# Performance work log

Hardware: AMD Instinct MI355X
Metric: run time of the kernel (lower is better)

Reference implementation:

```python
import jax, jax.numpy as jnp
import numpy as np

T = 2048          # tokens (single causal prefill sequence)
H = 4096          # hidden_size
NH = 32           # num query heads
NKV = 8           # num kv heads (GQA)
HD = H // NH      # head_dim = 128
ROPE_THETA = 500000.0
Q_SIZE = NH * HD
KV_SIZE = NKV * HD


def setup_inputs() -> dict:
    key = jax.random.key(0)
    k1, k2, k3 = jax.random.split(key, 3)
    return {
        "positions": jnp.arange(T, dtype=jnp.int32),
        "hidden_states": jax.random.normal(k1, (T, H), dtype=jnp.float32) * 0.02,
        "w_qkv": jax.random.normal(k2, (H, Q_SIZE + 2 * KV_SIZE), dtype=jnp.float32) * (1.0 / np.sqrt(H)),
        "w_o": jax.random.normal(k3, (Q_SIZE, H), dtype=jnp.float32) * (1.0 / np.sqrt(Q_SIZE)),
    }


def _apply_rope(x, positions):
    # x: [T, heads, HD]; neox-style (non-interleaved) RoPE as in get_rope
    half = HD // 2
    inv_freq = 1.0 / (ROPE_THETA ** (jnp.arange(0, half, dtype=jnp.float32) / half * 1.0))
    # note: standard llama uses arange(0, HD, 2)/HD == arange(half)/half
    freqs = positions.astype(jnp.float32)[:, None] * inv_freq[None, :]   # [T, half]
    cos = jnp.cos(freqs)[:, None, :]  # [T, 1, half]
    sin = jnp.sin(freqs)[:, None, :]
    x1, x2 = x[..., :half], x[..., half:]
    return jnp.concatenate([x1 * cos - x2 * sin, x2 * cos + x1 * sin], axis=-1).astype(x.dtype)


def reference(positions, hidden_states, w_qkv, w_o):
    # qkv_proj (no bias)
    qkv = hidden_states @ w_qkv                               # [T, 6144]
    q, k, v = jnp.split(qkv, [Q_SIZE, Q_SIZE + KV_SIZE], axis=-1)
    q = q.reshape(T, NH, HD)
    k = k.reshape(T, NKV, HD)
    v = v.reshape(T, NKV, HD)

    # fused RoPE on q and k (k would be written rotated into the KV cache)
    q = _apply_rope(q, positions)
    k = _apply_rope(k, positions)

    # GQA: expand kv heads to query heads
    group = NH // NKV
    k_rep = jnp.repeat(k, group, axis=1)                      # [T, NH, HD]
    v_rep = jnp.repeat(v, group, axis=1)

    scale = HD ** -0.5
    scores = jnp.einsum('qhd,shd->hqs', q, k_rep) * scale     # [NH, T, T]
    causal = jnp.tril(jnp.ones((T, T), dtype=bool))
    scores = jnp.where(causal[None], scores, jnp.finfo(scores.dtype).min)
    probs = jax.nn.softmax(scores, axis=-1)
    attn = jnp.einsum('hqs,shd->qhd', probs, v_rep)           # [T, NH, HD]

    out = attn.reshape(T, Q_SIZE) @ w_o                       # o_proj
    return out
```

## Files before the change

kernel.cpp:

```cpp
#include <hip/hip_runtime.h>
#include <cstdint>
#include <cstddef>

#define T_SEQ 2048
#define H_DIM 4096
#define NH 32
#define NKV 8
#define HD 128
#define QKV_N 6144
#define Q_SIZE 4096
#define KV_SIZE 1024

typedef __attribute__((ext_vector_type(8))) short bf16x8;
typedef __attribute__((ext_vector_type(4))) short short4v;
typedef __attribute__((ext_vector_type(4))) float f32x4;

__device__ __forceinline__ short f2bf(float f) {
  union { float f; uint32_t u; } v; v.f = f;
  uint32_t r = v.u + 0x7fffu + ((v.u >> 16) & 1u);
  return (short)(r >> 16);
}

__device__ __forceinline__ void gload_lds16(const void* g, void* l) {
  __builtin_amdgcn_global_load_lds((const __attribute__((address_space(1))) void*)g,
                                   (__attribute__((address_space(3))) void*)l,
                                   16, 0, 0);
}

__global__ __launch_bounds__(256) void cvt_bf16_kernel(const float* __restrict__ in,
                                                       short* __restrict__ out, int n4) {
  int i = blockIdx.x * 256 + threadIdx.x;
  if (i < n4) {
    float4 v = ((const float4*)in)[i];
    short4v s;
    s.x = f2bf(v.x); s.y = f2bf(v.y); s.z = f2bf(v.z); s.w = f2bf(v.w);
    ((short4v*)out)[i] = s;
  }
}

__global__ __launch_bounds__(256) void transpose_cvt_kernel(const float* __restrict__ in,
                                                            short* __restrict__ out,
                                                            int rows, int cols) {
  __shared__ float tile[32][33];
  int bx = blockIdx.x * 32;
  int by = blockIdx.y * 32;
  int x = threadIdx.x, y = threadIdx.y;
#pragma unroll
  for (int i = 0; i < 32; i += 8)
    tile[y + i][x] = in[(size_t)(by + y + i) * cols + bx + x];
  __syncthreads();
#pragma unroll
  for (int i = 0; i < 32; i += 8)
    out[(size_t)(bx + y + i) * rows + by + x] = f2bf(tile[x][y + i]);
}

#define BARRIER() do { __builtin_amdgcn_s_barrier(); \
                       __builtin_amdgcn_sched_barrier(0); \
                       asm volatile("" ::: "memory"); } while (0)
#define VMCNT4() asm volatile("s_waitcnt vmcnt(4)" ::: "memory")
#define PRIO1 __builtin_amdgcn_s_setprio(1)
#define PRIO0 __builtin_amdgcn_s_setprio(0)

#define LDA_HALF(BASE, MH) do { \
  _Pragma("unroll") \
  for (int m_ = 0; m_ < 4; ++m_) { \
    _Pragma("unroll") \
    for (int ks_ = 0; ks_ < 2; ++ks_) { \
      int row_ = arow + (MH) * 64 + m_ * 16 + l16; \
      aF[m_][ks_] = *(const bf16x8*)((BASE) + row_ * 64 + (((ks_ * 4 + quad) ^ (row_ & 7)) << 3)); \
    } } } while (0)

#define LDB_HALF(BASE, NH, DST) do { \
  _Pragma("unroll") \
  for (int n_ = 0; n_ < 2; ++n_) { \
    _Pragma("unroll") \
    for (int ks_ = 0; ks_ < 2; ++ks_) { \
      int row_ = brow + (NH) * 32 + n_ * 16 + l16; \
      (DST)[n_][ks_] = *(const bf16x8*)((BASE) + row_ * 64 + (((ks_ * 4 + quad) ^ (row_ & 7)) << 3)); \
    } } } while (0)

#define MMQ(MH, NH, BF) do { \
  _Pragma("unroll") \
  for (int m_ = 0; m_ < 4; ++m_) { \
    _Pragma("unroll") \
    for (int n_ = 0; n_ < 2; ++n_) { \
      _Pragma("unroll") \
      for (int ks_ = 0; ks_ < 2; ++ks_) \
        acc[(MH) * 4 + m_][(NH) * 2 + n_] = __builtin_amdgcn_mfma_f32_16x16x32_bf16( \
            aF[m_][ks_], (BF)[n_][ks_], acc[(MH) * 4 + m_][(NH) * 2 + n_], 0, 0, 0); \
    } } } while (0)

__device__ __forceinline__ void stage_half(const short* __restrict__ src, int ldk,
                                           short* dst, int half, int tid) {
#pragma unroll
  for (int q = 0; q < 2; ++q) {
    int cc = half * 1024 + q * 512 + tid;
    int row = cc >> 3, cq = cc & 7;
    gload_lds16(src + (size_t)row * ldk + ((cq ^ (row & 7)) << 3), dst + cc * 8);
  }
}

__global__ __launch_bounds__(512, 1) void gemm_bt256_kernel(const short* __restrict__ A,
                                                            const short* __restrict__ Bt,
                                                            float* __restrict__ C,
                                                            int M, int N, int K) {
  __shared__ short lds[65536];
  short* As0 = lds;
  short* Bs0 = lds + 16384;
  short* As1 = lds + 32768;
  short* Bs1 = lds + 49152;
  int tid = threadIdx.x;
  int w = tid >> 6, lane = tid & 63;
  int quad = lane >> 4, l16 = lane & 15;
  int wr = w >> 2, wc = w & 3;
  int arow = wr * 128, brow = wc * 64;
  int bm = blockIdx.y * 256, bn = blockIdx.x * 256;
  const short* Asrc = A + (size_t)bm * K;
  const short* Bsrc = Bt + (size_t)bn * K;
  int NT = K >> 6, NI = NT >> 1;

  f32x4 acc[8][4] = {};
  bf16x8 aF[4][2], b0F[2][2], b1F[2][2];

  stage_half(Asrc, K, As0, 0, tid);
  stage_half(Asrc, K, As0, 1, tid);
  stage_half(Bsrc, K, Bs0, 0, tid);
  stage_half(Bsrc, K, Bs0, 1, tid);
  stage_half(Bsrc + 64, K, Bs1, 0, tid);
  stage_half(Bsrc + 64, K, Bs1, 1, tid);
  VMCNT4();
  BARRIER();

#pragma unroll 1
  for (int i = 0; i < NI; ++i) {
    const short* a1 = Asrc + (size_t)(2 * i + 1) * 64;
    int kt2 = 2 * i + 2; if (kt2 > NT - 1) kt2 = NT - 1;
    int kt3 = 2 * i + 3; if (kt3 > NT - 1) kt3 = NT - 1;
    const short* a2 = Asrc + (size_t)kt2 * 64;
    const short* b2 = Bsrc + (size_t)kt2 * 64;
    const short* b3 = Bsrc + (size_t)kt3 * 64;

    LDA_HALF(As0, 0);
    LDB_HALF(Bs0, 0, b0F);
    stage_half(a1, K, As1, 0, tid);
    BARRIER();
    PRIO1; MMQ(0, 0, b0F); PRIO0;
    BARRIER();
    LDB_HALF(Bs0, 1, b1F);
    stage_half(a1, K, As1, 1, tid);
    BARRIER();
    PRIO1; MMQ(0, 1, b1F); PRIO0;
    BARRIER();
    LDA_HALF(As0, 1);
    stage_half(b2, K, Bs0, 0, tid);
    BARRIER();
    PRIO1; MMQ(1, 1, b1F); PRIO0;
    BARRIER();
    stage_half(b2, K, Bs0, 1, tid);
    BARRIER();
    PRIO1; MMQ(1, 0, b0F); PRIO0;
    VMCNT4();
    BARRIER();
    LDA_HALF(As1, 0);
    LDB_HALF(Bs1, 0, b0F);
    stage_half(a2, K, As0, 0, tid);
    BARRIER();
    PRIO1; MMQ(0, 0, b0F); PRIO0;
    BARRIER();
    LDB_HALF(Bs1, 1, b1F);
    stage_half(a2, K, As0, 1, tid);
    BARRIER();
    PRIO1; MMQ(0, 1, b1F); PRIO0;
    BARRIER();
    LDA_HALF(As1, 1);
    stage_half(b3, K, Bs1, 0, tid);
    BARRIER();
    PRIO1; MMQ(1, 1, b1F); PRIO0;
    BARRIER();
    stage_half(b3, K, Bs1, 1, tid);
    BARRIER();
    PRIO1; MMQ(1, 0, b0F); PRIO0;
    VMCNT4();
    BARRIER();
  }
  asm volatile("s_waitcnt vmcnt(0)" ::: "memory");

#pragma unroll
  for (int mi = 0; mi < 8; ++mi)
#pragma unroll
    for (int ni = 0; ni < 4; ++ni) {
      int r0 = bm + arow + mi * 16 + quad * 4;
      int c0 = bn + brow + ni * 16 + l16;
#pragma unroll
      for (int r = 0; r < 4; ++r)
        C[(size_t)(r0 + r) * N + c0] = acc[mi][ni][r];
    }
}

__global__ __launch_bounds__(256) void rope_kernel(const float* __restrict__ qkv,
                                                   const int* __restrict__ positions,
                                                   short* __restrict__ qb,
                                                   short* __restrict__ kb) {
  int t = blockIdx.x;
  int hh = blockIdx.y * 4 + (threadIdx.x >> 6);
  int j = threadIdx.x & 63;
  float pos = (float)positions[t];
  float f = pos * exp2f(-(float)j * 0.29580575889569017f);
  float c = cosf(f), sn = sinf(f);
  size_t rowbase = (size_t)t * QKV_N;
  int coloff = (hh < NH) ? hh * HD : Q_SIZE + (hh - NH) * HD;
  float x1 = qkv[rowbase + coloff + j];
  float x2 = qkv[rowbase + coloff + j + 64];
  float o1 = x1 * c - x2 * sn;
  float o2 = x2 * c + x1 * sn;
  const float scale2 = 0.08838834764831845f * 1.4426950408889634f;
  short* dst;
  if (hh < NH) {
    o1 *= scale2; o2 *= scale2;
    dst = qb + ((size_t)hh * T_SEQ + t) * HD;
  } else {
    dst = kb + ((size_t)(hh - NH) * T_SEQ + t) * HD;
  }
  dst[j] = f2bf(o1);
  dst[j + 64] = f2bf(o2);
}

__global__ __launch_bounds__(256) void transpose_v_kernel(const float* __restrict__ qkv,
                                                          short* __restrict__ vt) {
  __shared__ float tile[32][33];
  int bx = blockIdx.x * 32;
  int by = blockIdx.y * 32;
  int x = threadIdx.x, y = threadIdx.y;
#pragma unroll
  for (int i = 0; i < 32; i += 8)
    tile[y + i][x] = qkv[(size_t)(by + y + i) * QKV_N + (Q_SIZE + KV_SIZE) + bx + x];
  __syncthreads();
#pragma unroll
  for (int i = 0; i < 32; i += 8)
    vt[(size_t)(bx + y + i) * T_SEQ + by + x] = f2bf(tile[x][y + i]);
}

#define PS_STR 72
__global__ __launch_bounds__(256, 2) void flash_kernel(const short* __restrict__ qb,
                                                       const short* __restrict__ kb,
                                                       const short* __restrict__ vt,
                                                       short* __restrict__ attn) {
  __shared__ short Ks[64 * 128];
  __shared__ short Vs[128 * 64];
  __shared__ short Ps[8][16 * PS_STR];
  int c = (int)gridDim.x - 1 - (int)blockIdx.x;
  int h = blockIdx.y;
  int kvh = h >> 2;
  int tid = threadIdx.x;
  int w = tid >> 6, lane = tid & 63;
  int quad = lane >> 4, l16 = lane & 15;
  int qrow0w = c * 128 + w * 32;

  const short* kbh = kb + (size_t)kvh * T_SEQ * HD;
  const short* vth = vt + (size_t)kvh * HD * T_SEQ;

  bf16x8 qf[2][4];
#pragma unroll
  for (int g = 0; g < 2; ++g) {
    const short* qbase = qb + ((size_t)h * T_SEQ + qrow0w + g * 16 + l16) * HD + quad * 8;
#pragma unroll
    for (int dk = 0; dk < 4; ++dk) qf[g][dk] = *(const bf16x8*)(qbase + dk * 32);
  }
  f32x4 o[2][8] = {};
  float lp[2] = {0.0f, 0.0f};

  int ktmax_blk = 2 * c + 2;
  int ktmax_w = 2 * c + 1 + (w >> 1);

  for (int kt = 0; kt < ktmax_blk; ++kt) {
    int kpos0 = kt * 64;
    __syncthreads();
#pragma unroll
    for (int p4 = 0; p4 < 4; ++p4) {
      int e = p4 * 256 + tid;
      int kr = e >> 4, kp = e & 15;
      gload_lds16(kbh + (size_t)(kpos0 + kr) * HD + ((kp ^ (kr & 7)) * 8), Ks + e * 8);
      int vd = e >> 3, vp = e & 7;
      gload_lds16(vth + (size_t)vd * T_SEQ + kpos0 + ((vp ^ (vd & 7)) * 8), Vs + e * 8);
    }
    __syncthreads();
    if (kt >= ktmax_w) continue;

    f32x4 s[2][4] = {};
#pragma unroll
    for (int mi = 0; mi < 4; ++mi) {
      int kr = mi * 16 + l16;
      const short* kfb = Ks + kr * 128;
      int sw = kr & 7;
#pragma unroll
      for (int dk = 0; dk < 4; ++dk) {
        bf16x8 kf = *(const bf16x8*)(kfb + (((dk * 4 + quad) ^ sw) * 8));
        s[0][mi] = __builtin_amdgcn_mfma_f32_16x16x32_bf16(kf, qf[0][dk], s[0][mi], 0, 0, 0);
        s[1][mi] = __builtin_amdgcn_mfma_f32_16x16x32_bf16(kf, qf[1][dk], s[1][mi], 0, 0, 0);
      }
    }
#pragma unroll
    for (int g = 0; g < 2; ++g) {
      int qr = qrow0w + g * 16 + l16;
      bool need_mask = (kpos0 + 63 > qrow0w + g * 16);
#pragma unroll
      for (int mi = 0; mi < 4; ++mi) {
        float p0, p1, p2, p3;
        if (need_mask) {
          int kp = kpos0 + mi * 16 + quad * 4;
          p0 = exp2f((kp + 0 > qr) ? -1e30f : s[g][mi][0]);
          p1 = exp2f((kp + 1 > qr) ? -1e30f : s[g][mi][1]);
          p2 = exp2f((kp + 2 > qr) ? -1e30f : s[g][mi][2]);
          p3 = exp2f((kp + 3 > qr) ? -1e30f : s[g][mi][3]);
        } else {
          p0 = exp2f(s[g][mi][0]); p1 = exp2f(s[g][mi][1]);
          p2 = exp2f(s[g][mi][2]); p3 = exp2f(s[g][mi][3]);
        }
        lp[g] += p0 + p1 + p2 + p3;
        short4v pk;
        pk.x = f2bf(p0); pk.y = f2bf(p1); pk.z = f2bf(p2); pk.w = f2bf(p3);
        *(short4v*)(&Ps[w * 2 + g][l16 * PS_STR + mi * 16 + quad * 4]) = pk;
      }
    }
#pragma unroll
    for (int kf2 = 0; kf2 < 2; ++kf2) {
      bf16x8 pf0 = *(const bf16x8*)(&Ps[w * 2 + 0][l16 * PS_STR + kf2 * 32 + quad * 8]);
      bf16x8 pf1 = *(const bf16x8*)(&Ps[w * 2 + 1][l16 * PS_STR + kf2 * 32 + quad * 8]);
#pragma unroll
      for (int ni = 0; ni < 8; ++ni) {
        int vd = ni * 16 + l16;
        bf16x8 vf = *(const bf16x8*)(Vs + vd * 64 + (((kf2 * 4 + quad) ^ (vd & 7)) * 8));
        o[0][ni] = __builtin_amdgcn_mfma_f32_16x16x32_bf16(vf, pf0, o[0][ni], 0, 0, 0);
        o[1][ni] = __builtin_amdgcn_mfma_f32_16x16x32_bf16(vf, pf1, o[1][ni], 0, 0, 0);
      }
    }
  }
#pragma unroll
  for (int g = 0; g < 2; ++g) {
    float lt = lp[g];
    lt += __shfl_xor(lt, 16, 64);
    lt += __shfl_xor(lt, 32, 64);
    float rl = 1.0f / lt;
    short* dst = attn + (size_t)(qrow0w + g * 16 + l16) * Q_SIZE + h * HD + quad * 4;
#pragma unroll
    for (int ni = 0; ni < 8; ++ni) {
      short4v ov;
      ov.x = f2bf(o[g][ni][0] * rl); ov.y = f2bf(o[g][ni][1] * rl);
      ov.z = f2bf(o[g][ni][2] * rl); ov.w = f2bf(o[g][ni][3] * rl);
      *(short4v*)(dst + ni * 16) = ov;
    }
  }
}

extern "C" void kernel_launch(void* const* d_in, const int* in_sizes, int n_in,
                              void* d_out, int out_size, void* d_ws, size_t ws_size,
                              hipStream_t stream) {
  const int* positions = (const int*)d_in[0];
  const float* hidden  = (const float*)d_in[1];
  const float* w_qkv   = (const float*)d_in[2];
  const float* w_o     = (const float*)d_in[3];
  float* out = (float*)d_out;

  char* p = (char*)d_ws;
  short* hA    = (short*)p;               short* attn = hA;
  p += (size_t)T_SEQ * H_DIM * 2;
  short* wqkvT = (short*)p;
  p += (size_t)QKV_N * H_DIM * 2;
  float* qkv   = (float*)p;               short* woT = (short*)p;
  short* qb = wqkvT;
  short* kb = qb + (size_t)NH * T_SEQ * HD;
  short* vt = kb + (size_t)NKV * T_SEQ * HD;

  cvt_bf16_kernel<<<dim3(T_SEQ * H_DIM / 4 / 256), 256, 0, stream>>>(hidden, hA, T_SEQ * H_DIM / 4);
  transpose_cvt_kernel<<<dim3(QKV_N / 32, H_DIM / 32), dim3(32, 8), 0, stream>>>(w_qkv, wqkvT, H_DIM, QKV_N);
  gemm_bt256_kernel<<<dim3(QKV_N / 256, T_SEQ / 256), 512, 0, stream>>>(hA, wqkvT, qkv, T_SEQ, QKV_N, H_DIM);
  rope_kernel<<<dim3(T_SEQ, (NH + NKV) / 4), 256, 0, stream>>>(qkv, positions, qb, kb);
  transpose_v_kernel<<<dim3(KV_SIZE / 32, T_SEQ / 32), dim3(32, 8), 0, stream>>>(qkv, vt);
  transpose_cvt_kernel<<<dim3(H_DIM / 32, H_DIM / 32), dim3(32, 8), 0, stream>>>(w_o, woT, H_DIM, H_DIM);
  flash_kernel<<<dim3(T_SEQ / 128, NH), 256, 0, stream>>>(qb, kb, vt, attn);
  gemm_bt256_kernel<<<dim3(H_DIM / 256, T_SEQ / 256), 512, 0, stream>>>(attn, woT, out, T_SEQ, H_DIM, H_DIM);
}
```

Measured before the change: 543.0 us.

## Split-K the o_proj GEMM with atomics and widen weight transpose tiles

The o_proj GEMM grid had only 128 blocks (16x8) on a device with far more CUs. It now splits K in two, zeroes the output first and accumulates with float atomicAdd, doubling the block count. The weight transpose-convert kernel also moves to 64x64 tiles with float4 loads and 16-byte bf16 stores. The trade-off is an extra zeroing pass and atomic write traffic, plus non-deterministic summation order.

```diff
diff --git a/kernel.cpp b/kernel.cpp
--- a/kernel.cpp
+++ b/kernel.cpp
@@ -38,20 +38,41 @@
   }
 }
 
-__global__ __launch_bounds__(256) void transpose_cvt_kernel(const float* __restrict__ in,
-                                                            short* __restrict__ out,
-                                                            int rows, int cols) {
-  __shared__ float tile[32][33];
-  int bx = blockIdx.x * 32;
-  int by = blockIdx.y * 32;
-  int x = threadIdx.x, y = threadIdx.y;
-#pragma unroll
-  for (int i = 0; i < 32; i += 8)
-    tile[y + i][x] = in[(size_t)(by + y + i) * cols + bx + x];
+__global__ __launch_bounds__(256) void zero_f4_kernel(float* __restrict__ p, int n4) {
+  int i = blockIdx.x * 256 + threadIdx.x;
+  int stride = gridDim.x * 256;
+  float4 z = {0.f, 0.f, 0.f, 0.f};
+  for (; i < n4; i += stride) ((float4*)p)[i] = z;
+}
+
+__global__ __launch_bounds__(256) void transpose_cvt64_kernel(const float* __restrict__ in,
+                                                              short* __restrict__ out,
+                                                              int rows, int cols) {
+  __shared__ float tile[64][65];
+  int bx = blockIdx.x * 64;
+  int by = blockIdx.y * 64;
+  int t = threadIdx.x;
+  int lr = t >> 4;
+  int lc4 = t & 15;
+#pragma unroll
+  for (int p = 0; p < 4; ++p) {
+    int r = p * 16 + lr;
+    float4 v = *(const float4*)(in + (size_t)(by + r) * cols + bx + lc4 * 4);
+    tile[r][lc4 * 4 + 0] = v.x; tile[r][lc4 * 4 + 1] = v.y;
+    tile[r][lc4 * 4 + 2] = v.z; tile[r][lc4 * 4 + 3] = v.w;
+  }
   __syncthreads();
-#pragma unroll
-  for (int i = 0; i < 32; i += 8)
-    out[(size_t)(bx + y + i) * rows + by + x] = f2bf(tile[x][y + i]);
+  int w = t >> 6, l = t & 63;
+  int colg = l >> 3;
+  int rseg = (l & 7) * 8;
+#pragma unroll
+  for (int p = 0; p < 2; ++p) {
+    int col = (p * 4 + w) * 8 + colg;
+    bf16x8 r8;
+#pragma unroll
+    for (int i = 0; i < 8; ++i) r8[i] = f2bf(tile[rseg + i][col]);
+    *(bf16x8*)(out + (size_t)(bx + col) * rows + by + rseg) = r8;
+  }
 }
 
 #define BARRIER() do { __builtin_amdgcn_s_barrier(); \
@@ -103,7 +124,8 @@
 __global__ __launch_bounds__(512, 1) void gemm_bt256_kernel(const short* __restrict__ A,
                                                             const short* __restrict__ Bt,
                                                             float* __restrict__ C,
-                                                            int M, int N, int K) {
+                                                            int M, int N, int K,
+                                                            int klen) {
   __shared__ short lds[65536];
   short* As0 = lds;
   short* Bs0 = lds + 16384;
@@ -115,9 +137,10 @@
   int wr = w >> 2, wc = w & 3;
   int arow = wr * 128, brow = wc * 64;
   int bm = blockIdx.y * 256, bn = blockIdx.x * 256;
-  const short* Asrc = A + (size_t)bm * K;
-  const short* Bsrc = Bt + (size_t)bn * K;
-  int NT = K >> 6, NI = NT >> 1;
+  int k0 = blockIdx.z * klen;
+  const short* Asrc = A + (size_t)bm * K + k0;
+  const short* Bsrc = Bt + (size_t)bn * K + k0;
+  int NT = klen >> 6, NI = NT >> 1;
 
   f32x4 acc[8][4] = {};
   bf16x8 aF[4][2], b0F[2][2], b1F[2][2];
@@ -185,16 +208,29 @@
   }
   asm volatile("s_waitcnt vmcnt(0)" ::: "memory");
 
-#pragma unroll
-  for (int mi = 0; mi < 8; ++mi)
-#pragma unroll
-    for (int ni = 0; ni < 4; ++ni) {
-      int r0 = bm + arow + mi * 16 + quad * 4;
-      int c0 = bn + brow + ni * 16 + l16;
-#pragma unroll
-      for (int r = 0; r < 4; ++r)
-        C[(size_t)(r0 + r) * N + c0] = acc[mi][ni][r];
-    }
+  if (gridDim.z > 1) {
+#pragma unroll
+    for (int mi = 0; mi < 8; ++mi)
+#pragma unroll
+      for (int ni = 0; ni < 4; ++ni) {
+        int r0 = bm + arow + mi * 16 + quad * 4;
+        int c0 = bn + brow + ni * 16 + l16;
+#pragma unroll
+        for (int r = 0; r < 4; ++r)
+          atomicAdd(&C[(size_t)(r0 + r) * N + c0], acc[mi][ni][r]);
+      }
+  } else {
+#pragma unroll
+    for (int mi = 0; mi < 8; ++mi)
+#pragma unroll
+      for (int ni = 0; ni < 4; ++ni) {
+        int r0 = bm + arow + mi * 16 + quad * 4;
+        int c0 = bn + brow + ni * 16 + l16;
+#pragma unroll
+        for (int r = 0; r < 4; ++r)
+          C[(size_t)(r0 + r) * N + c0] = acc[mi][ni][r];
+      }
+  }
 }
 
 __global__ __launch_bounds__(256) void rope_kernel(const float* __restrict__ qkv,
@@ -372,11 +408,12 @@
   short* vt = kb + (size_t)NKV * T_SEQ * HD;
 
   cvt_bf16_kernel<<<dim3(T_SEQ * H_DIM / 4 / 256), 256, 0, stream>>>(hidden, hA, T_SEQ * H_DIM / 4);
-  transpose_cvt_kernel<<<dim3(QKV_N / 32, H_DIM / 32), dim3(32, 8), 0, stream>>>(w_qkv, wqkvT, H_DIM, QKV_N);
-  gemm_bt256_kernel<<<dim3(QKV_N / 256, T_SEQ / 256), 512, 0, stream>>>(hA, wqkvT, qkv, T_SEQ, QKV_N, H_DIM);
+  transpose_cvt64_kernel<<<dim3(QKV_N / 64, H_DIM / 64), 256, 0, stream>>>(w_qkv, wqkvT, H_DIM, QKV_N);
+  gemm_bt256_kernel<<<dim3(QKV_N / 256, T_SEQ / 256, 1), 512, 0, stream>>>(hA, wqkvT, qkv, T_SEQ, QKV_N, H_DIM, H_DIM);
   rope_kernel<<<dim3(T_SEQ, (NH + NKV) / 4), 256, 0, stream>>>(qkv, positions, qb, kb);
   transpose_v_kernel<<<dim3(KV_SIZE / 32, T_SEQ / 32), dim3(32, 8), 0, stream>>>(qkv, vt);
-  transpose_cvt_kernel<<<dim3(H_DIM / 32, H_DIM / 32), dim3(32, 8), 0, stream>>>(w_o, woT, H_DIM, H_DIM);
+  transpose_cvt64_kernel<<<dim3(H_DIM / 64, H_DIM / 64), 256, 0, stream>>>(w_o, woT, H_DIM, H_DIM);
   flash_kernel<<<dim3(T_SEQ / 128, NH), 256, 0, stream>>>(qb, kb, vt, attn);
-  gemm_bt256_kernel<<<dim3(H_DIM / 256, T_SEQ / 256), 512, 0, stream>>>(attn, woT, out, T_SEQ, H_DIM, H_DIM);
-}
+  zero_f4_kernel<<<dim3(2048), 256, 0, stream>>>(out, T_SEQ * H_DIM / 4);
+  gemm_bt256_kernel<<<dim3(H_DIM / 256, T_SEQ / 256, 2), 512, 0, stream>>>(attn, woT, out, T_SEQ, H_DIM, H_DIM, H_DIM / 2);
+}
```

Measured after the change: 545.0 us. About the same (+0.4%).
